# Performance work log

Hardware: AMD Instinct MI355X
Metric: run time of the kernel (lower is better)

Reference implementation:

```python
import jax, jax.numpy as jnp
import numpy as np

# Static graph / model sizes (closed over; match input_specs)
N0, N1, N2 = 500_000, 100_000, 25_000   # nodes per hop (targets are prefix of sources)
E0, E1 = 1_600_000, 400_000             # edges per hop
D_IN, D_H, D_OUT = 128, 256, 128


def setup_inputs() -> dict:
    key = jax.random.key(0)
    ks = jax.random.split(key, 11)
    s_in = 1.0 / np.sqrt(D_IN)
    s_h = 1.0 / np.sqrt(D_H)
    return {
        "x": jax.random.normal(ks[0], (N0, D_IN), dtype=jnp.float32),
        # layer 0 params (SAGEConv in->hidden): lin_l (with bias) on aggregated, lin_r (no bias) on root
        "W_l0": jax.random.normal(ks[1], (D_H, D_IN), dtype=jnp.float32) * s_in,
        "b_l0": jax.random.normal(ks[2], (D_H,), dtype=jnp.float32) * s_in,
        "W_r0": jax.random.normal(ks[3], (D_H, D_IN), dtype=jnp.float32) * s_in,
        # layer 1 params (SAGEConv hidden->out)
        "W_l1": jax.random.normal(ks[4], (D_OUT, D_H), dtype=jnp.float32) * s_h,
        "b_l1": jax.random.normal(ks[5], (D_OUT,), dtype=jnp.float32) * s_h,
        "W_r1": jax.random.normal(ks[6], (D_OUT, D_H), dtype=jnp.float32) * s_h,
        # bipartite edge indices: src in [0, N_src), dst in [0, N_dst)
        "ei0_src": jax.random.randint(ks[7], (E0,), 0, N0),
        "ei0_dst": jax.random.randint(ks[8], (E0,), 0, N1),
        "ei1_src": jax.random.randint(ks[9], (E1,), 0, N1),
        "ei1_dst": jax.random.randint(ks[10], (E1,), 0, N2),
    }


def _sage_conv(x_src, x_dst, src, dst, n_dst, W_l, b_l, W_r):
    """PyG SAGEConv, aggr='mean': lin_l(mean_neigh) + lin_r(x_dst)."""
    msg = x_src[src]                                                # [E, d] gather
    agg = jax.ops.segment_sum(msg, dst, num_segments=n_dst)        # [n_dst, d]
    cnt = jax.ops.segment_sum(jnp.ones((src.shape[0],), msg.dtype), dst,
                              num_segments=n_dst)                  # [n_dst]
    agg = agg / jnp.clip(cnt, 1.0)[:, None]                        # mean (safe for isolated nodes)
    return agg @ W_l.T + b_l + x_dst @ W_r.T


def reference(x, W_l0, b_l0, W_r0, W_l1, b_l1, W_r1,
              ei0_src, ei0_dst, ei1_src, ei1_dst):
    # hop 0: targets are first N1 rows of x
    h = _sage_conv(x, x[:N1], ei0_src, ei0_dst, N1, W_l0, b_l0, W_r0)
    h = jax.nn.relu(h)  # relu on all but last layer
    # hop 1 (last layer, no relu)
    out = _sage_conv(h, h[:N2], ei1_src, ei1_dst, N2, W_l1, b_l1, W_r1)
    return out
```

## Files before the change

### kernel.cpp

```cpp
#include <hip/hip_runtime.h>
#include <hip/hip_bf16.h>

#define cN0 500000
#define cN1 100000
#define cN2 25000
#define cE0 1600000
#define cE1 400000

typedef __bf16 bf16x8 __attribute__((ext_vector_type(8)));
typedef __bf16 bf16x4 __attribute__((ext_vector_type(4)));
typedef float f32x4 __attribute__((ext_vector_type(4)));


__global__ void k_hist(const int* __restrict__ dst, int E, int* __restrict__ cnt) {
    int i = blockIdx.x * blockDim.x + threadIdx.x;
    if (i < E) atomicAdd(&cnt[dst[i]], 1);
}

__global__ void k_scan1(int* __restrict__ a, int n, int* __restrict__ bsum) {
    __shared__ int lds[256];
    const int t = threadIdx.x;
    const int base = blockIdx.x * 1024 + t * 4;
    int v0 = (base + 0 < n) ? a[base + 0] : 0;
    int v1 = (base + 1 < n) ? a[base + 1] : 0;
    int v2 = (base + 2 < n) ? a[base + 2] : 0;
    int v3 = (base + 3 < n) ? a[base + 3] : 0;
    const int s = v0 + v1 + v2 + v3;
    lds[t] = s;
    __syncthreads();
    int x = s;
    for (int d = 1; d < 256; d <<= 1) {
        int y = (t >= d) ? lds[t - d] : 0;
        __syncthreads();
        x += y;
        lds[t] = x;
        __syncthreads();
    }
    if (t == 255) bsum[blockIdx.x] = x;
    int e0 = x - s;
    int e1 = e0 + v0, e2 = e1 + v1, e3 = e2 + v2;
    if (base + 0 < n) a[base + 0] = e0;
    if (base + 1 < n) a[base + 1] = e1;
    if (base + 2 < n) a[base + 2] = e2;
    if (base + 3 < n) a[base + 3] = e3;
}

__global__ void k_scan2(int* __restrict__ bsum, int nb) {
    __shared__ int lds[128];
    const int t = threadIdx.x;
    int v = (t < nb) ? bsum[t] : 0;
    lds[t] = v;
    __syncthreads();
    int x = v;
    for (int d = 1; d < 128; d <<= 1) {
        int y = (t >= d) ? lds[t - d] : 0;
        __syncthreads();
        x += y;
        lds[t] = x;
        __syncthreads();
    }
    if (t < nb) bsum[t] = x - v;
}

__global__ void k_scan3(int* __restrict__ a, int n, const int* __restrict__ bsum, int total,
                        int* __restrict__ cur) {
    int i = blockIdx.x * blockDim.x + threadIdx.x;
    if (i < n) {
        int v = a[i] + bsum[i >> 10];
        a[i] = v;
        cur[i] = v;
    }
    if (i == 0) a[n] = total;
}

__global__ void k_scatter(const int* __restrict__ esrc, const int* __restrict__ edst, int E,
                          int* __restrict__ cur, int* __restrict__ srcs) {
    int i = blockIdx.x * blockDim.x + threadIdx.x;
    if (i < E) {
        int p = atomicAdd(&cur[edst[i]], 1);
        srcs[p] = esrc[i];
    }
}

__global__ void k_wcat0(const float* __restrict__ Wl, const float* __restrict__ Wr,
                        __bf16* __restrict__ Wc) {
    int i = blockIdx.x * blockDim.x + threadIdx.x;
    if (i < 256 * 256) {
        int j = i >> 8, k = i & 255;
        float v = (k < 128) ? Wl[j * 128 + k] : Wr[j * 128 + (k - 128)];
        Wc[i] = (__bf16)v;
    }
}
__global__ void k_wcat1(const float* __restrict__ Wl, const float* __restrict__ Wr,
                        __bf16* __restrict__ Wc) {
    int i = blockIdx.x * blockDim.x + threadIdx.x;
    if (i < 128 * 512) {
        int j = i >> 9, k = i & 511;
        float v = (k < 256) ? Wl[j * 256 + k] : Wr[j * 256 + (k - 256)];
        Wc[i] = (__bf16)v;
    }
}

__global__ __launch_bounds__(256) void k_cast(const float* __restrict__ x,
                                              __bf16* __restrict__ xb,
                                              __bf16* __restrict__ M0) {
    const size_t t = (size_t)blockIdx.x * 256 + threadIdx.x;
    const size_t base = t * 8;
    const f32x4 a = __builtin_nontemporal_load((const f32x4*)(x + base));
    const f32x4 b = __builtin_nontemporal_load((const f32x4*)(x + base + 4));
    bf16x8 o;
    o[0] = (__bf16)a[0]; o[1] = (__bf16)a[1]; o[2] = (__bf16)a[2]; o[3] = (__bf16)a[3];
    o[4] = (__bf16)b[0]; o[5] = (__bf16)b[1]; o[6] = (__bf16)b[2]; o[7] = (__bf16)b[3];
    *(bf16x8*)(xb + base) = o;
    const int row = (int)(base >> 7);
    if (row < cN1) {
        const int col = (int)(base & 127);
        *(bf16x8*)(M0 + (size_t)row * 256 + 128 + col) = o;
    }
}

__global__ __launch_bounds__(256) void k_agg0(
    const __bf16* __restrict__ xb,
    const int* __restrict__ off, const int* __restrict__ srcs,
    __bf16* __restrict__ M0)
{
    const int tid = threadIdx.x;
    const int slot = tid >> 5;
    const int ln = tid & 31;
    const int g = blockIdx.x * 8 + slot;
    if (g >= cN1) return;
    const int e0 = off[g], e1 = off[g + 1];
    float a0 = 0.f, a1 = 0.f, a2 = 0.f, a3 = 0.f;
    int e = e0;
    for (; e + 4 <= e1; e += 4) {
        const int s0 = srcs[e], s1 = srcs[e + 1], s2 = srcs[e + 2], s3 = srcs[e + 3];
        const bf16x4 r0 = *(const bf16x4*)(xb + (size_t)s0 * 128 + ln * 4);
        const bf16x4 r1 = *(const bf16x4*)(xb + (size_t)s1 * 128 + ln * 4);
        const bf16x4 r2 = *(const bf16x4*)(xb + (size_t)s2 * 128 + ln * 4);
        const bf16x4 r3 = *(const bf16x4*)(xb + (size_t)s3 * 128 + ln * 4);
        a0 += ((float)r0[0] + (float)r1[0]) + ((float)r2[0] + (float)r3[0]);
        a1 += ((float)r0[1] + (float)r1[1]) + ((float)r2[1] + (float)r3[1]);
        a2 += ((float)r0[2] + (float)r1[2]) + ((float)r2[2] + (float)r3[2]);
        a3 += ((float)r0[3] + (float)r1[3]) + ((float)r2[3] + (float)r3[3]);
    }
    for (; e < e1; ++e) {
        const int s = srcs[e];
        const bf16x4 r = *(const bf16x4*)(xb + (size_t)s * 128 + ln * 4);
        a0 += (float)r[0]; a1 += (float)r[1]; a2 += (float)r[2]; a3 += (float)r[3];
    }
    const int cnt = e1 - e0;
    const float inv = 1.f / (float)(cnt > 0 ? cnt : 1);
    bf16x4 oa;
    oa[0] = (__bf16)(a0 * inv); oa[1] = (__bf16)(a1 * inv);
    oa[2] = (__bf16)(a2 * inv); oa[3] = (__bf16)(a3 * inv);
    *(bf16x4*)(M0 + (size_t)g * 256 + ln * 4) = oa;
}

__global__ __launch_bounds__(256) void k_agg1(
    const __bf16* __restrict__ h,
    const int* __restrict__ off, const int* __restrict__ srcs,
    __bf16* __restrict__ M1)
{
    const int tid = threadIdx.x;
    const int wave = tid >> 6;
    const int lane = tid & 63;
    const int g = blockIdx.x * 4 + wave;
    if (g >= cN2) return;
    const int e0 = off[g], e1 = off[g + 1];
    float a0 = 0.f, a1 = 0.f, a2 = 0.f, a3 = 0.f;
    int e = e0;
    for (; e + 4 <= e1; e += 4) {
        const int s0 = srcs[e], s1 = srcs[e + 1], s2 = srcs[e + 2], s3 = srcs[e + 3];
        const bf16x4 r0 = *(const bf16x4*)(h + (size_t)s0 * 256 + lane * 4);
        const bf16x4 r1 = *(const bf16x4*)(h + (size_t)s1 * 256 + lane * 4);
        const bf16x4 r2 = *(const bf16x4*)(h + (size_t)s2 * 256 + lane * 4);
        const bf16x4 r3 = *(const bf16x4*)(h + (size_t)s3 * 256 + lane * 4);
        a0 += (float)r0[0] + (float)r1[0] + (float)r2[0] + (float)r3[0];
        a1 += (float)r0[1] + (float)r1[1] + (float)r2[1] + (float)r3[1];
        a2 += (float)r0[2] + (float)r1[2] + (float)r2[2] + (float)r3[2];
        a3 += (float)r0[3] + (float)r1[3] + (float)r2[3] + (float)r3[3];
    }
    for (; e < e1; ++e) {
        const int s = srcs[e];
        const bf16x4 r = *(const bf16x4*)(h + (size_t)s * 256 + lane * 4);
        a0 += (float)r[0]; a1 += (float)r[1]; a2 += (float)r[2]; a3 += (float)r[3];
    }
    const int cnt = e1 - e0;
    const float inv = 1.f / (float)(cnt > 0 ? cnt : 1);
    bf16x4 oa;
    oa[0] = (__bf16)(a0 * inv); oa[1] = (__bf16)(a1 * inv);
    oa[2] = (__bf16)(a2 * inv); oa[3] = (__bf16)(a3 * inv);
    *(bf16x4*)(M1 + (size_t)g * 512 + lane * 4) = oa;
    *(bf16x4*)(M1 + (size_t)g * 512 + 256 + lane * 4) =
        *(const bf16x4*)(h + (size_t)g * 256 + lane * 4);
}

template<int K, int LDC, bool RELU, bool OUTBF16>
__global__ __launch_bounds__(256) void k_gemm(
    const __bf16* __restrict__ Mm, const __bf16* __restrict__ W,
    const float* __restrict__ bias,
    float* __restrict__ outf, __bf16* __restrict__ outb, int Mrows)
{
    const int tid = threadIdx.x;
    const int l = tid & 63;
    const int w = tid >> 6;
    const int wm = w & 1, wn = w >> 1;
    const int row0 = blockIdx.x * 128 + wm * 64;
    const int col0 = blockIdx.y * 128 + wn * 64;
    const int lr = l & 15;
    const int lk = (l >> 4) * 8;

    const __bf16* pa[4];
    const __bf16* pb[4];
    #pragma unroll
    for (int i = 0; i < 4; ++i) {
        int r = row0 + i * 16 + lr;
        r = (r < Mrows) ? r : (Mrows - 1);
        pa[i] = Mm + (size_t)r * K + lk;
        pb[i] = W + (size_t)(col0 + i * 16 + lr) * K + lk;
    }
    f32x4 acc[4][4];
    #pragma unroll
    for (int i = 0; i < 4; ++i)
        #pragma unroll
        for (int j = 0; j < 4; ++j)
            acc[i][j] = (f32x4)0.0f;

    #pragma unroll 2
    for (int k0 = 0; k0 < K; k0 += 32) {
        bf16x8 fa[4], fb[4];
        #pragma unroll
        for (int i = 0; i < 4; ++i) fa[i] = *(const bf16x8*)(pa[i] + k0);
        #pragma unroll
        for (int j = 0; j < 4; ++j) fb[j] = *(const bf16x8*)(pb[j] + k0);
        #pragma unroll
        for (int i = 0; i < 4; ++i)
            #pragma unroll
            for (int j = 0; j < 4; ++j)
                acc[i][j] = __builtin_amdgcn_mfma_f32_16x16x32_bf16(fa[i], fb[j], acc[i][j], 0, 0, 0);
    }

    #pragma unroll
    for (int j = 0; j < 4; ++j) {
        const int colg = col0 + j * 16 + lr;
        const float bj = bias[colg];
        #pragma unroll
        for (int i = 0; i < 4; ++i) {
            #pragma unroll
            for (int reg = 0; reg < 4; ++reg) {
                const int rowg = row0 + i * 16 + (l >> 4) * 4 + reg;
                if (rowg < Mrows) {
                    float v = acc[i][j][reg] + bj;
                    if (RELU) v = fmaxf(v, 0.f);
                    if (OUTBF16) outb[(size_t)rowg * LDC + colg] = (__bf16)v;
                    else         outf[(size_t)rowg * LDC + colg] = v;
                }
            }
        }
    }
}


extern "C" void kernel_launch(void* const* d_in, const int* in_sizes, int n_in,
                              void* d_out, int out_size, void* d_ws, size_t ws_size,
                              hipStream_t stream) {
    const float* x   = (const float*)d_in[0];
    const float* Wl0 = (const float*)d_in[1];
    const float* bl0 = (const float*)d_in[2];
    const float* Wr0 = (const float*)d_in[3];
    const float* Wl1 = (const float*)d_in[4];
    const float* bl1 = (const float*)d_in[5];
    const float* Wr1 = (const float*)d_in[6];
    const int* e0s = (const int*)d_in[7];
    const int* e0d = (const int*)d_in[8];
    const int* e1s = (const int*)d_in[9];
    const int* e1d = (const int*)d_in[10];
    float* out = (float*)d_out;

    char* ws = (char*)d_ws;
    size_t pos = 0;
    auto alloc = [&](size_t nb) -> void* {
        void* p = ws + pos;
        pos += (nb + 255) & ~(size_t)255;
        return p;
    };
    __bf16* xb   = (__bf16*)alloc((size_t)cN0 * 128 * 2);
    __bf16* h    = xb;
    __bf16* M0   = (__bf16*)alloc((size_t)cN1 * 256 * 2);
    __bf16* M1   = M0;
    int* off0    = (int*)alloc((size_t)(cN1 + 1) * 4);
    int* cur0    = (int*)alloc((size_t)cN1 * 4);
    int* srcs0   = (int*)alloc((size_t)cE0 * 4);
    int* off1    = (int*)alloc((size_t)(cN2 + 1) * 4);
    int* cur1    = (int*)alloc((size_t)cN2 * 4);
    int* srcs1   = (int*)alloc((size_t)cE1 * 4);
    int* bsum    = (int*)alloc(128 * 4);
    __bf16* Wc0  = (__bf16*)alloc(256 * 256 * 2);
    __bf16* Wc1  = (__bf16*)alloc(128 * 512 * 2);
    (void)ws_size; (void)in_sizes; (void)n_in; (void)out_size;

    hipMemsetAsync(off0, 0, (size_t)(cN1 + 1) * 4, stream);
    hipMemsetAsync(off1, 0, (size_t)(cN2 + 1) * 4, stream);
    k_hist<<<(cE0 + 255) / 256, 256, 0, stream>>>(e0d, cE0, off0);
    k_hist<<<(cE1 + 255) / 256, 256, 0, stream>>>(e1d, cE1, off1);

    const int nb0 = (cN1 + 1023) / 1024;
    k_scan1<<<nb0, 256, 0, stream>>>(off0, cN1, bsum);
    k_scan2<<<1, 128, 0, stream>>>(bsum, nb0);
    k_scan3<<<(cN1 + 255) / 256, 256, 0, stream>>>(off0, cN1, bsum, cE0, cur0);
    k_scatter<<<(cE0 + 255) / 256, 256, 0, stream>>>(e0s, e0d, cE0, cur0, srcs0);

    const int nb1 = (cN2 + 1023) / 1024;
    k_scan1<<<nb1, 256, 0, stream>>>(off1, cN2, bsum);
    k_scan2<<<1, 128, 0, stream>>>(bsum, nb1);
    k_scan3<<<(cN2 + 255) / 256, 256, 0, stream>>>(off1, cN2, bsum, cE1, cur1);
    k_scatter<<<(cE1 + 255) / 256, 256, 0, stream>>>(e1s, e1d, cE1, cur1, srcs1);

    k_wcat0<<<(256 * 256 + 255) / 256, 256, 0, stream>>>(Wl0, Wr0, Wc0);
    k_wcat1<<<(128 * 512 + 255) / 256, 256, 0, stream>>>(Wl1, Wr1, Wc1);

    k_cast<<<(cN0 * 128 / 8) / 256, 256, 0, stream>>>(x, xb, M0);

    k_agg0<<<(cN1 + 7) / 8, 256, 0, stream>>>(xb, off0, srcs0, M0);
    {
        dim3 grid((cN1 + 127) / 128, 2);
        k_gemm<256, 256, true, true><<<grid, 256, 0, stream>>>(M0, Wc0, bl0, nullptr, h, cN1);
    }
    k_agg1<<<(cN2 + 3) / 4, 256, 0, stream>>>(h, off1, srcs1, M1);
    {
        dim3 grid((cN2 + 127) / 128, 1);
        k_gemm<512, 128, false, false><<<grid, 256, 0, stream>>>(M1, Wc1, bl1, out, nullptr, cN2);
    }
}
```

Measured before the change: 816.7 us.

## Merge per-hop CSR build kernels and widen layer-0 GEMM tile to full N

```diff
diff --git a/kernel.cpp b/kernel.cpp
--- a/kernel.cpp
+++ b/kernel.cpp
@@ -12,15 +12,25 @@
 typedef float f32x4 __attribute__((ext_vector_type(4)));
 
 
-__global__ void k_hist(const int* __restrict__ dst, int E, int* __restrict__ cnt) {
+__global__ void k_hist(const int* __restrict__ d0, const int* __restrict__ d1,
+                       int* __restrict__ c0, int* __restrict__ c1) {
     int i = blockIdx.x * blockDim.x + threadIdx.x;
-    if (i < E) atomicAdd(&cnt[dst[i]], 1);
-}
-
-__global__ void k_scan1(int* __restrict__ a, int n, int* __restrict__ bsum) {
+    if (i < cE0) {
+        atomicAdd(&c0[d0[i]], 1);
+    } else {
+        int j = i - cE0;
+        if (j < cE1) atomicAdd(&c1[d1[j]], 1);
+    }
+}
+
+__global__ void k_scan1(int* __restrict__ a0, int* __restrict__ a1, int nb0,
+                        int* __restrict__ bsum) {
     __shared__ int lds[256];
     const int t = threadIdx.x;
-    const int base = blockIdx.x * 1024 + t * 4;
+    int* a; int n; int* bs; int bb;
+    if ((int)blockIdx.x < nb0) { a = a0; n = cN1; bs = bsum;       bb = blockIdx.x; }
+    else                       { a = a1; n = cN2; bs = bsum + 128; bb = blockIdx.x - nb0; }
+    const int base = bb * 1024 + t * 4;
     int v0 = (base + 0 < n) ? a[base + 0] : 0;
     int v1 = (base + 1 < n) ? a[base + 1] : 0;
     int v2 = (base + 2 < n) ? a[base + 2] : 0;
@@ -36,7 +46,7 @@
         lds[t] = x;
         __syncthreads();
     }
-    if (t == 255) bsum[blockIdx.x] = x;
+    if (t == 255) bs[bb] = x;
     int e0 = x - s;
     int e1 = e0 + v0, e2 = e1 + v1, e3 = e2 + v2;
     if (base + 0 < n) a[base + 0] = e0;
@@ -45,10 +55,12 @@
     if (base + 3 < n) a[base + 3] = e3;
 }
 
-__global__ void k_scan2(int* __restrict__ bsum, int nb) {
+__global__ void k_scan2(int* __restrict__ bsum, int nb0, int nb1) {
     __shared__ int lds[128];
     const int t = threadIdx.x;
-    int v = (t < nb) ? bsum[t] : 0;
+    int* bs = bsum + blockIdx.x * 128;
+    const int nb = (blockIdx.x == 0) ? nb0 : nb1;
+    int v = (t < nb) ? bs[t] : 0;
     lds[t] = v;
     __syncthreads();
     int x = v;
@@ -59,45 +71,58 @@
         lds[t] = x;
         __syncthreads();
     }
-    if (t < nb) bsum[t] = x - v;
-}
-
-__global__ void k_scan3(int* __restrict__ a, int n, const int* __restrict__ bsum, int total,
-                        int* __restrict__ cur) {
+    if (t < nb) bs[t] = x - v;
+}
+
+__global__ void k_scan3(int* __restrict__ off0, int* __restrict__ off1,
+                        const int* __restrict__ bsum,
+                        int* __restrict__ cur0, int* __restrict__ cur1) {
     int i = blockIdx.x * blockDim.x + threadIdx.x;
-    if (i < n) {
-        int v = a[i] + bsum[i >> 10];
-        a[i] = v;
-        cur[i] = v;
-    }
-    if (i == 0) a[n] = total;
-}
-
-__global__ void k_scatter(const int* __restrict__ esrc, const int* __restrict__ edst, int E,
-                          int* __restrict__ cur, int* __restrict__ srcs) {
+    if (i < cN1) {
+        int v = off0[i] + bsum[i >> 10];
+        off0[i] = v;
+        cur0[i] = v;
+    }
+    if (i < cN2) {
+        int v = off1[i] + bsum[128 + (i >> 10)];
+        off1[i] = v;
+        cur1[i] = v;
+    }
+    if (i == 0) { off0[cN1] = cE0; off1[cN2] = cE1; }
+}
+
+__global__ void k_scatter(const int* __restrict__ e0s, const int* __restrict__ e0d,
+                          const int* __restrict__ e1s, const int* __restrict__ e1d,
+                          int* __restrict__ cur0, int* __restrict__ cur1,
+                          int* __restrict__ srcs0, int* __restrict__ srcs1) {
     int i = blockIdx.x * blockDim.x + threadIdx.x;
-    if (i < E) {
-        int p = atomicAdd(&cur[edst[i]], 1);
-        srcs[p] = esrc[i];
-    }
-}
-
-__global__ void k_wcat0(const float* __restrict__ Wl, const float* __restrict__ Wr,
-                        __bf16* __restrict__ Wc) {
+    if (i < cE0) {
+        int p = atomicAdd(&cur0[e0d[i]], 1);
+        srcs0[p] = e0s[i];
+    } else {
+        int j = i - cE0;
+        if (j < cE1) {
+            int p = atomicAdd(&cur1[e1d[j]], 1);
+            srcs1[p] = e1s[j];
+        }
+    }
+}
+
+__global__ void k_wcat(const float* __restrict__ Wl0, const float* __restrict__ Wr0,
+                       const float* __restrict__ Wl1, const float* __restrict__ Wr1,
+                       __bf16* __restrict__ Wc0, __bf16* __restrict__ Wc1) {
     int i = blockIdx.x * blockDim.x + threadIdx.x;
     if (i < 256 * 256) {
         int j = i >> 8, k = i & 255;
-        float v = (k < 128) ? Wl[j * 128 + k] : Wr[j * 128 + (k - 128)];
-        Wc[i] = (__bf16)v;
-    }
-}
-__global__ void k_wcat1(const float* __restrict__ Wl, const float* __restrict__ Wr,
-                        __bf16* __restrict__ Wc) {
-    int i = blockIdx.x * blockDim.x + threadIdx.x;
-    if (i < 128 * 512) {
-        int j = i >> 9, k = i & 511;
-        float v = (k < 256) ? Wl[j * 256 + k] : Wr[j * 256 + (k - 256)];
-        Wc[i] = (__bf16)v;
+        float v = (k < 128) ? Wl0[j * 128 + k] : Wr0[j * 128 + (k - 128)];
+        Wc0[i] = (__bf16)v;
+    } else {
+        int i2 = i - 256 * 256;
+        if (i2 < 128 * 512) {
+            int j = i2 >> 9, k = i2 & 511;
+            float v = (k < 256) ? Wl1[j * 256 + k] : Wr1[j * 256 + (k - 256)];
+            Wc1[i2] = (__bf16)v;
+        }
     }
 }
 
@@ -195,7 +220,7 @@
         *(const bf16x4*)(h + (size_t)g * 256 + lane * 4);
 }
 
-template<int K, int LDC, bool RELU, bool OUTBF16>
+template<int K, int LDC, int NJ, int UNR, bool RELU, bool OUTBF16>
 __global__ __launch_bounds__(256) void k_gemm(
     const __bf16* __restrict__ Mm, const __bf16* __restrict__ W,
     const float* __restrict__ bias,
@@ -206,42 +231,45 @@
     const int w = tid >> 6;
     const int wm = w & 1, wn = w >> 1;
     const int row0 = blockIdx.x * 128 + wm * 64;
-    const int col0 = blockIdx.y * 128 + wn * 64;
+    const int col0 = blockIdx.y * (NJ * 32) + wn * (NJ * 16);
     const int lr = l & 15;
     const int lk = (l >> 4) * 8;
 
     const __bf16* pa[4];
-    const __bf16* pb[4];
+    const __bf16* pb[NJ];
     #pragma unroll
     for (int i = 0; i < 4; ++i) {
         int r = row0 + i * 16 + lr;
         r = (r < Mrows) ? r : (Mrows - 1);
         pa[i] = Mm + (size_t)r * K + lk;
-        pb[i] = W + (size_t)(col0 + i * 16 + lr) * K + lk;
-    }
-    f32x4 acc[4][4];
+    }
+    #pragma unroll
+    for (int j = 0; j < NJ; ++j)
+        pb[j] = W + (size_t)(col0 + j * 16 + lr) * K + lk;
+
+    f32x4 acc[4][NJ];
     #pragma unroll
     for (int i = 0; i < 4; ++i)
         #pragma unroll
-        for (int j = 0; j < 4; ++j)
+        for (int j = 0; j < NJ; ++j)
             acc[i][j] = (f32x4)0.0f;
 
-    #pragma unroll 2
+    #pragma unroll UNR
     for (int k0 = 0; k0 < K; k0 += 32) {
-        bf16x8 fa[4], fb[4];
+        bf16x8 fa[4], fb[NJ];
         #pragma unroll
         for (int i = 0; i < 4; ++i) fa[i] = *(const bf16x8*)(pa[i] + k0);
         #pragma unroll
-        for (int j = 0; j < 4; ++j) fb[j] = *(const bf16x8*)(pb[j] + k0);
+        for (int j = 0; j < NJ; ++j) fb[j] = *(const bf16x8*)(pb[j] + k0);
         #pragma unroll
         for (int i = 0; i < 4; ++i)
             #pragma unroll
-            for (int j = 0; j < 4; ++j)
+            for (int j = 0; j < NJ; ++j)
                 acc[i][j] = __builtin_amdgcn_mfma_f32_16x16x32_bf16(fa[i], fb[j], acc[i][j], 0, 0, 0);
     }
 
     #pragma unroll
-    for (int j = 0; j < 4; ++j) {
+    for (int j = 0; j < NJ; ++j) {
         const int colg = col0 + j * 16 + lr;
         const float bj = bias[colg];
         #pragma unroll
@@ -288,47 +316,40 @@
     __bf16* h    = xb;
     __bf16* M0   = (__bf16*)alloc((size_t)cN1 * 256 * 2);
     __bf16* M1   = M0;
-    int* off0    = (int*)alloc((size_t)(cN1 + 1) * 4);
+    int* off0    = (int*)alloc((size_t)(cN1 + 1 + cN2 + 1) * 4);
+    int* off1    = off0 + (cN1 + 1);
     int* cur0    = (int*)alloc((size_t)cN1 * 4);
+    int* cur1    = (int*)alloc((size_t)cN2 * 4);
     int* srcs0   = (int*)alloc((size_t)cE0 * 4);
-    int* off1    = (int*)alloc((size_t)(cN2 + 1) * 4);
-    int* cur1    = (int*)alloc((size_t)cN2 * 4);
     int* srcs1   = (int*)alloc((size_t)cE1 * 4);
-    int* bsum    = (int*)alloc(128 * 4);
+    int* bsum    = (int*)alloc(256 * 4);
     __bf16* Wc0  = (__bf16*)alloc(256 * 256 * 2);
     __bf16* Wc1  = (__bf16*)alloc(128 * 512 * 2);
     (void)ws_size; (void)in_sizes; (void)n_in; (void)out_size;
 
-    hipMemsetAsync(off0, 0, (size_t)(cN1 + 1) * 4, stream);
-    hipMemsetAsync(off1, 0, (size_t)(cN2 + 1) * 4, stream);
-    k_hist<<<(cE0 + 255) / 256, 256, 0, stream>>>(e0d, cE0, off0);
-    k_hist<<<(cE1 + 255) / 256, 256, 0, stream>>>(e1d, cE1, off1);
-
     const int nb0 = (cN1 + 1023) / 1024;
-    k_scan1<<<nb0, 256, 0, stream>>>(off0, cN1, bsum);
-    k_scan2<<<1, 128, 0, stream>>>(bsum, nb0);
-    k_scan3<<<(cN1 + 255) / 256, 256, 0, stream>>>(off0, cN1, bsum, cE0, cur0);
-    k_scatter<<<(cE0 + 255) / 256, 256, 0, stream>>>(e0s, e0d, cE0, cur0, srcs0);
-
     const int nb1 = (cN2 + 1023) / 1024;
-    k_scan1<<<nb1, 256, 0, stream>>>(off1, cN2, bsum);
-    k_scan2<<<1, 128, 0, stream>>>(bsum, nb1);
-    k_scan3<<<(cN2 + 255) / 256, 256, 0, stream>>>(off1, cN2, bsum, cE1, cur1);
-    k_scatter<<<(cE1 + 255) / 256, 256, 0, stream>>>(e1s, e1d, cE1, cur1, srcs1);
-
-    k_wcat0<<<(256 * 256 + 255) / 256, 256, 0, stream>>>(Wl0, Wr0, Wc0);
-    k_wcat1<<<(128 * 512 + 255) / 256, 256, 0, stream>>>(Wl1, Wr1, Wc1);
+
+    hipMemsetAsync(off0, 0, (size_t)(cN1 + 1 + cN2 + 1) * 4, stream);
+    k_hist<<<(cE0 + cE1 + 255) / 256, 256, 0, stream>>>(e0d, e1d, off0, off1);
+    k_scan1<<<nb0 + nb1, 256, 0, stream>>>(off0, off1, nb0, bsum);
+    k_scan2<<<2, 128, 0, stream>>>(bsum, nb0, nb1);
+    k_scan3<<<(cN1 + 255) / 256, 256, 0, stream>>>(off0, off1, bsum, cur0, cur1);
+    k_scatter<<<(cE0 + cE1 + 255) / 256, 256, 0, stream>>>(e0s, e0d, e1s, e1d,
+                                                           cur0, cur1, srcs0, srcs1);
+
+    k_wcat<<<(256 * 256 + 128 * 512 + 255) / 256, 256, 0, stream>>>(Wl0, Wr0, Wl1, Wr1, Wc0, Wc1);
 
     k_cast<<<(cN0 * 128 / 8) / 256, 256, 0, stream>>>(x, xb, M0);
 
     k_agg0<<<(cN1 + 7) / 8, 256, 0, stream>>>(xb, off0, srcs0, M0);
     {
-        dim3 grid((cN1 + 127) / 128, 2);
-        k_gemm<256, 256, true, true><<<grid, 256, 0, stream>>>(M0, Wc0, bl0, nullptr, h, cN1);
+        dim3 grid((cN1 + 127) / 128, 1);
+        k_gemm<256, 256, 8, 1, true, true><<<grid, 256, 0, stream>>>(M0, Wc0, bl0, nullptr, h, cN1);
     }
     k_agg1<<<(cN2 + 3) / 4, 256, 0, stream>>>(h, off1, srcs1, M1);
     {
         dim3 grid((cN2 + 127) / 128, 1);
-        k_gemm<512, 128, false, false><<<grid, 256, 0, stream>>>(M1, Wc1, bl1, out, nullptr, cN2);
-    }
-}
+        k_gemm<512, 128, 4, 2, false, false><<<grid, 256, 0, stream>>>(M1, Wc1, bl1, out, nullptr, cN2);
+    }
+}
```

New measurement: 871.8 us. +6.8%, slower.
